# Performance work log

Hardware: AMD Instinct MI355X
Metric: run time of the kernel (lower is better)

## Reference

```python
import jax, jax.numpy as jnp
import numpy as np

B, S, D_MODEL, H = 4, 2048, 1024, 16
DEPTH = D_MODEL // H  # 64


def setup_inputs() -> dict:
    key = jax.random.key(0)
    ks = jax.random.split(key, 12)
    inp = {
        "v": jax.random.normal(ks[0], (B, S, D_MODEL), jnp.float32),
        "k": jax.random.normal(ks[1], (B, S, D_MODEL), jnp.float32),
        "q": jax.random.normal(ks[2], (B, S, D_MODEL), jnp.float32),
        "mask": jnp.zeros((B, 1, 1, S), jnp.int32),  # unused by the layer
        # Dense(d_model) params (glorot-ish scale)
        "wq": jax.random.normal(ks[3], (D_MODEL, D_MODEL), jnp.float32) / np.sqrt(D_MODEL),
        "bq": jnp.zeros((D_MODEL,), jnp.float32),
        "wk": jax.random.normal(ks[4], (D_MODEL, D_MODEL), jnp.float32) / np.sqrt(D_MODEL),
        "bk": jnp.zeros((D_MODEL,), jnp.float32),
        "wv": jax.random.normal(ks[5], (D_MODEL, D_MODEL), jnp.float32) / np.sqrt(D_MODEL),
        "bv": jnp.zeros((D_MODEL,), jnp.float32),
        # global attention weights: [max_seq_len, 1], stddev=0.1
        "gqw": 0.1 * jax.random.normal(ks[6], (S, 1), jnp.float32),
        "gkw": 0.1 * jax.random.normal(ks[7], (S, 1), jnp.float32),
        "wo": jax.random.normal(ks[8], (D_MODEL, D_MODEL), jnp.float32) / np.sqrt(D_MODEL),
        "bo": jnp.zeros((D_MODEL,), jnp.float32),
    }
    return inp


def _split_heads(x):
    # [B, S, D] -> [B, H, S, depth]
    Bc = x.shape[0]
    return x.reshape(Bc, -1, H, DEPTH).transpose(0, 2, 1, 3)


def reference(v, k, q, mask, wq, bq, wk, bk, wv, bv, gqw, gkw, wo, bo):
    # QKV projections
    qh = _split_heads(q @ wq + bq)  # [B, H, S, depth]
    kh = _split_heads(k @ wk + bk)
    vh = _split_heads(v @ wv + bv)
    # Fastformer additive attention: mul -> seq-sum -> mul -> seq-sum -> mul -> add
    qh = qh * gqw                          # gqw [S,1] broadcasts over [B,H,S,depth]
    gq = jnp.sum(qh, axis=2, keepdims=True)  # global query [B,H,1,depth]
    kh = kh * gq * gkw
    gk = jnp.sum(kh, axis=2, keepdims=True)  # global key [B,H,1,depth]
    out = vh * gk + qh                       # [B,H,S,depth]
    # merge heads and output projection
    out = out.transpose(0, 2, 1, 3).reshape(out.shape[0], -1, D_MODEL)
    return out @ wo + bo
```

## Files before the change

### kernel.cpp

```cpp
#include <hip/hip_runtime.h>

#define DM 1024
#define BATCH 4
#define SEQ 2048
#define M_TOT (BATCH*SEQ)

typedef unsigned short ushort_t;
typedef __bf16 bf16x8 __attribute__((ext_vector_type(8)));
typedef float f32x4 __attribute__((ext_vector_type(4)));
typedef unsigned short u16x4 __attribute__((ext_vector_type(4)));
typedef unsigned short u16x8 __attribute__((ext_vector_type(8)));

__device__ __forceinline__ ushort_t f2bf(float f) {
  unsigned u = __builtin_bit_cast(unsigned, f);
  u = (u + 0x7fffu + ((u >> 16) & 1u)) >> 16;
  return (ushort_t)u;
}
__device__ __forceinline__ float bf2f(ushort_t h) {
  unsigned u = ((unsigned)h) << 16;
  return __builtin_bit_cast(float, u);
}

#define GLL(gp, lp)                                                            \
  __builtin_amdgcn_global_load_lds(                                            \
      (const __attribute__((address_space(1))) unsigned int*)(const void*)(gp),\
      (__attribute__((address_space(3))) unsigned int*)(void*)(lp), 16, 0, 0)

__global__ void k_reduce(const float* __restrict__ q, const float* __restrict__ k,
                         const float* __restrict__ v,
                         const float* __restrict__ gqw, const float* __restrict__ gkw,
                         float* __restrict__ pq, float* __restrict__ pk,
                         float* __restrict__ G,
                         ushort_t* __restrict__ qb, ushort_t* __restrict__ vb) {
  const int b = blockIdx.x, sc = blockIdx.y;
  const int d0 = threadIdx.x * 4;
  const int s0 = sc * 8;
  const size_t base = ((size_t)b * SEQ + s0) * DM + d0;
  float aq0 = 0.f, aq1 = 0.f, aq2 = 0.f, aq3 = 0.f;
  float ak0 = 0.f, ak1 = 0.f, ak2 = 0.f, ak3 = 0.f;
  float sgq = 0.f, sgk = 0.f;
#pragma unroll
  for (int i = 0; i < 8; ++i) {
    const float wq_ = gqw[s0 + i], wk_ = gkw[s0 + i];
    const size_t off = base + (size_t)i * DM;
    const float4 qv = *(const float4*)(q + off);
    const float4 kv = *(const float4*)(k + off);
    const float4 vv = *(const float4*)(v + off);
    aq0 += wq_ * qv.x; aq1 += wq_ * qv.y; aq2 += wq_ * qv.z; aq3 += wq_ * qv.w;
    ak0 += wk_ * kv.x; ak1 += wk_ * kv.y; ak2 += wk_ * kv.z; ak3 += wk_ * kv.w;
    u16x4 oq, ov;
    oq[0] = f2bf(wq_ * qv.x); oq[1] = f2bf(wq_ * qv.y);
    oq[2] = f2bf(wq_ * qv.z); oq[3] = f2bf(wq_ * qv.w);
    ov[0] = f2bf(vv.x); ov[1] = f2bf(vv.y); ov[2] = f2bf(vv.z); ov[3] = f2bf(vv.w);
    *(u16x4*)(qb + off) = oq;
    *(u16x4*)(vb + off) = ov;
    sgq += wq_; sgk += wk_;
  }
  const size_t po = ((size_t)(sc * BATCH + b) << 10) + d0;
  *(float4*)(pq + po) = make_float4(aq0, aq1, aq2, aq3);
  *(float4*)(pk + po) = make_float4(ak0, ak1, ak2, ak3);
  if (b == 0 && threadIdx.x == 0) {
    atomicAdd(&G[0], sgq);
    atomicAdd(&G[1], sgk);
  }
}

__global__ void k_rsum(const float* __restrict__ pq, const float* __restrict__ pk,
                       float* __restrict__ qr, float* __restrict__ kr) {
  const int b = blockIdx.x;
  const int d = blockIdx.y * 256 + threadIdx.x;
  const int sg = blockIdx.z;
  float aq = 0.f, ak = 0.f;
#pragma unroll 4
  for (int s = sg * 32; s < sg * 32 + 32; ++s) {
    const size_t po = ((size_t)(s * BATCH + b) << 10) + d;
    aq += pq[po];
    ak += pk[po];
  }
  atomicAdd(&qr[b * DM + d], aq);
  atomicAdd(&kr[b * DM + d], ak);
}

__global__ void k_gpart(const float* __restrict__ wq, const float* __restrict__ wk,
                        const float* __restrict__ qr, const float* __restrict__ kr,
                        float* __restrict__ qacc, float* __restrict__ kacc) {
  const int d = blockIdx.x * 256 + threadIdx.x;
  const int k0 = blockIdx.y * 32;
  __shared__ float sq[4][32], sk[4][32];
  if (threadIdx.x < 128) {
    const int b = threadIdx.x >> 5, kk = threadIdx.x & 31;
    sq[b][kk] = qr[b * DM + k0 + kk];
    sk[b][kk] = kr[b * DM + k0 + kk];
  }
  __syncthreads();
  float aq[4] = {0.f, 0.f, 0.f, 0.f}, ak[4] = {0.f, 0.f, 0.f, 0.f};
#pragma unroll 8
  for (int kk = 0; kk < 32; ++kk) {
    const float wqv = wq[(size_t)(k0 + kk) * DM + d];
    const float wkv = wk[(size_t)(k0 + kk) * DM + d];
#pragma unroll
    for (int b = 0; b < 4; ++b) {
      aq[b] += sq[b][kk] * wqv;
      ak[b] += sk[b][kk] * wkv;
    }
  }
#pragma unroll
  for (int b = 0; b < 4; ++b) {
    atomicAdd(&qacc[b * DM + d], aq[b]);
    atomicAdd(&kacc[b * DM + d], ak[b]);
  }
}

__global__ void k_gfin(const float* __restrict__ qacc, const float* __restrict__ kacc,
                       const float* __restrict__ bq, const float* __restrict__ bk,
                       const float* __restrict__ G, float* __restrict__ gk) {
  const int i = blockIdx.x * 256 + threadIdx.x;
  const int d = i & (DM - 1);
  const float gqv = qacc[i] + bq[d] * G[0];
  const float gkr = kacc[i] + bk[d] * G[1];
  gk[i] = gqv * gkr;
}

__global__ void k_conv(const float* __restrict__ x0, ushort_t* __restrict__ y0,
                       const float* __restrict__ x1, ushort_t* __restrict__ y1) {
  const float* x = blockIdx.y ? x1 : x0;
  ushort_t* y = blockIdx.y ? y1 : y0;
  size_t i = (size_t)blockIdx.x * 256 + threadIdx.x;
  const float4* p = (const float4*)x + i * 2;
  float4 a = p[0], b = p[1];
  u16x8 o;
  o[0] = f2bf(a.x); o[1] = f2bf(a.y); o[2] = f2bf(a.z); o[3] = f2bf(a.w);
  o[4] = f2bf(b.x); o[5] = f2bf(b.y); o[6] = f2bf(b.z); o[7] = f2bf(b.w);
  *(u16x8*)(y + i * 8) = o;
}

__global__ void k_trans(const float* __restrict__ W, ushort_t* __restrict__ T) {
  __shared__ float ls[32][33];
  const int bi = blockIdx.x, bj = blockIdx.y;
#pragma unroll
  for (int p = 0; p < 4; ++p) {
    int e = threadIdx.x + p * 256;
    int r = e >> 5, c = e & 31;
    ls[r][c] = W[(size_t)(bi * 32 + r) * DM + bj * 32 + c];
  }
  __syncthreads();
#pragma unroll
  for (int p = 0; p < 4; ++p) {
    int e = threadIdx.x + p * 256;
    int r = e >> 5, c = e & 31;
    T[(size_t)(bj * 32 + r) * DM + bi * 32 + c] = f2bf(ls[c][r]);
  }
}

__global__ void k_wog(const ushort_t* __restrict__ woT, const float* __restrict__ gk,
                      ushort_t* __restrict__ wogT) {
  const size_t i = (size_t)blockIdx.x * 256 + threadIdx.x;
  const size_t c = i * 8;
  const int j0 = (int)(c & (DM - 1));
  const int b = (int)(c >> 20);
  u16x8 wv = *(const u16x8*)(woT + (c & ((1u << 20) - 1)));
  const float4 g0 = *(const float4*)(gk + b * DM + j0);
  const float4 g1 = *(const float4*)(gk + b * DM + j0 + 4);
  float g[8] = {g0.x, g0.y, g0.z, g0.w, g1.x, g1.y, g1.z, g1.w};
  u16x8 o;
#pragma unroll
  for (int j = 0; j < 8; ++j) o[j] = f2bf(bf2f(wv[j]) * g[j]);
  *(u16x8*)(wogT + i * 8) = o;
}

__global__ void k_bias(const float* __restrict__ wo, const float* __restrict__ bq,
                       const float* __restrict__ bv, const float* __restrict__ gk,
                       float* __restrict__ qbias, float* __restrict__ vbias) {
  const int n = blockIdx.x * 256 + threadIdx.x;
  const int k0 = blockIdx.y * 32;
  float aq = 0.f, av[4] = {0.f, 0.f, 0.f, 0.f};
  for (int kk = 0; kk < 32; ++kk) {
    const float w = wo[(size_t)(k0 + kk) * DM + n];
    aq += bq[k0 + kk] * w;
    const float bw = bv[k0 + kk] * w;
#pragma unroll
    for (int b = 0; b < 4; ++b) av[b] += bw * gk[b * DM + k0 + kk];
  }
  atomicAdd(&qbias[n], aq);
#pragma unroll
  for (int b = 0; b < 4; ++b) atomicAdd(&vbias[b * DM + n], av[b]);
}

template <int MODE, int NT>
__global__ __launch_bounds__(512, 1)
void k_pipe(const ushort_t* __restrict__ A0, const ushort_t* __restrict__ B0,
            const ushort_t* __restrict__ A1, const ushort_t* __restrict__ B1,
            const float* __restrict__ gqw, const float* __restrict__ qbias,
            const float* __restrict__ vbias, const float* __restrict__ bo,
            void* __restrict__ OutV) {
  __shared__ __align__(16) ushort_t lsA[3][256 * 64];
  __shared__ __align__(16) ushort_t lsB[3][128 * 64];
  const int tid = threadIdx.x;
  const int w = tid >> 6, lane = tid & 63;
  const int m0 = blockIdx.x * 256, n0 = blockIdx.y * 128;
  const int b = (MODE == 0) ? (m0 >> 11) : 0;
  const int wr = w >> 2, wc = w & 3;

  const ushort_t *Aq, *Bq, *Av = nullptr, *Bv = nullptr;
  if constexpr (MODE == 0) {
    Aq = A0; Bq = B0; Av = A1; Bv = B1 + (size_t)b * (DM * DM);
  } else {
    const int z = blockIdx.z;
    Aq = z ? A1 + (size_t)(z - 1) * (DM * DM) : A0;
    Bq = z ? B1 : B0;
  }

  const int subrow = lane >> 3;
  const int srcslot = (lane & 7) ^ subrow;
  size_t offA[4], offB[2];
#pragma unroll
  for (int p = 0; p < 4; ++p) {
    const int row = (4 * w + p) * 8 + subrow;
    offA[p] = (size_t)(m0 + row) * DM + srcslot * 8;
  }
#pragma unroll
  for (int p = 0; p < 2; ++p) {
    const int row = (2 * w + p) * 8 + subrow;
    offB[p] = (size_t)(n0 + row) * DM + srcslot * 8;
  }

  const int g = lane >> 4, l7 = lane & 7, l15 = lane & 15;
  int aoff[2][8], boff[2][2];
#pragma unroll
  for (int kh = 0; kh < 2; ++kh) {
#pragma unroll
    for (int i = 0; i < 8; ++i) {
      const int ra = wr * 128 + i * 16 + l15;
      aoff[kh][i] = ra * 64 + (((kh * 4 + g) ^ l7) * 8);
    }
#pragma unroll
    for (int j = 0; j < 2; ++j) {
      const int rb = wc * 32 + j * 16 + l15;
      boff[kh][j] = rb * 64 + (((kh * 4 + g) ^ l7) * 8);
    }
  }

  f32x4 acc[8][2];
#pragma unroll
  for (int i = 0; i < 8; ++i)
#pragma unroll
    for (int j = 0; j < 2; ++j) acc[i][j] = (f32x4){0.f, 0.f, 0.f, 0.f};

  auto SRC = [&](int tt, const ushort_t*& Ab, const ushort_t*& Bb, int& k0) {
    if (MODE == 0 && tt >= NT / 2) { Ab = Av; Bb = Bv; k0 = (tt - NT / 2) * 64; }
    else                           { Ab = Aq; Bb = Bq; k0 = tt * 64; }
  };
  auto STAGE_H0 = [&](int tt, int buf) {
    const ushort_t *Ab, *Bb; int k0; SRC(tt, Ab, Bb, k0);
    GLL(Ab + offA[0] + k0, &lsA[buf][(4 * w + 0) * 512]);
    GLL(Ab + offA[1] + k0, &lsA[buf][(4 * w + 1) * 512]);
    GLL(Bb + offB[0] + k0, &lsB[buf][(2 * w + 0) * 512]);
  };
  auto STAGE_H1 = [&](int tt, int buf) {
    const ushort_t *Ab, *Bb; int k0; SRC(tt, Ab, Bb, k0);
    GLL(Ab + offA[2] + k0, &lsA[buf][(4 * w + 2) * 512]);
    GLL(Ab + offA[3] + k0, &lsA[buf][(4 * w + 3) * 512]);
    GLL(Bb + offB[1] + k0, &lsB[buf][(2 * w + 1) * 512]);
  };
  auto READF = [&](bf16x8 (&av)[8], bf16x8 (&bv)[2], int cur, int kh) {
#pragma unroll
    for (int i = 0; i < 8; ++i) av[i] = *(const bf16x8*)(&lsA[cur][aoff[kh][i]]);
#pragma unroll
    for (int j = 0; j < 2; ++j) bv[j] = *(const bf16x8*)(&lsB[cur][boff[kh][j]]);
  };
  auto DOMFMA = [&](bf16x8 (&av)[8], bf16x8 (&bv)[2]) {
    __builtin_amdgcn_s_setprio(1);
#pragma unroll
    for (int i = 0; i < 8; ++i)
#pragma unroll
      for (int j = 0; j < 2; ++j)
        acc[i][j] = __builtin_amdgcn_mfma_f32_16x16x32_bf16(av[i], bv[j], acc[i][j], 0, 0, 0);
    __builtin_amdgcn_s_setprio(0);
  };

  bf16x8 avA[8], bvA[2], avB[8], bvB[2];

  STAGE_H0(0, 0); STAGE_H1(0, 0);
  STAGE_H0(1, 1); STAGE_H1(1, 1);
  asm volatile("s_waitcnt vmcnt(6)" ::: "memory");
  __builtin_amdgcn_s_barrier();
  READF(avA, bvA, 0, 0);

#pragma unroll 1
  for (int t = 0; t < NT; ++t) {
    const int cur = t % 3, nb = (t + 2) % 3, nxt = (t + 1) % 3;
    READF(avB, bvB, cur, 1);
    if (t + 2 < NT) STAGE_H0(t + 2, nb);
    DOMFMA(avA, bvA);
    if (t + 1 < NT) {
      if (t + 2 < NT) { asm volatile("s_waitcnt vmcnt(3)\n\ts_barrier" ::: "memory"); }
      else            { asm volatile("s_waitcnt vmcnt(0)\n\ts_barrier" ::: "memory"); }
      READF(avA, bvA, nxt, 0);
      if (t + 2 < NT) STAGE_H1(t + 2, nb);
    }
    DOMFMA(avB, bvB);
  }

  const int lr = (lane >> 4) * 4, lc = lane & 15;
  const int rbase = m0 + wr * 128, cbase = n0 + wc * 32;
  if constexpr (MODE == 0) {
    float* Out = (float*)OutV;
#pragma unroll
    for (int j = 0; j < 2; ++j) {
      const int col = cbase + j * 16 + lc;
      const float qbn = qbias[col];
      const float cb = vbias[b * DM + col] + bo[col];
#pragma unroll
      for (int i = 0; i < 8; ++i)
#pragma unroll
        for (int r = 0; r < 4; ++r) {
          const int row = rbase + i * 16 + lr + r;
          Out[(size_t)row * DM + col] = acc[i][j][r] + gqw[row & (SEQ - 1)] * qbn + cb;
        }
    }
  } else {
    ushort_t* Out = (ushort_t*)OutV + (size_t)blockIdx.z * (DM * DM);
#pragma unroll
    for (int j = 0; j < 2; ++j) {
      const int col = cbase + j * 16 + lc;
#pragma unroll
      for (int i = 0; i < 8; ++i)
#pragma unroll
        for (int r = 0; r < 4; ++r) {
          const int row = rbase + i * 16 + lr + r;
          Out[(size_t)row * DM + col] = f2bf(acc[i][j][r]);
        }
    }
  }
}

extern "C" void kernel_launch(void* const* d_in, const int* in_sizes, int n_in,
                              void* d_out, int out_size, void* d_ws, size_t ws_size,
                              hipStream_t stream) {
  const float* v   = (const float*)d_in[0];
  const float* k   = (const float*)d_in[1];
  const float* q   = (const float*)d_in[2];
  const float* wq  = (const float*)d_in[4];
  const float* bq  = (const float*)d_in[5];
  const float* wk  = (const float*)d_in[6];
  const float* bk  = (const float*)d_in[7];
  const float* wv  = (const float*)d_in[8];
  const float* bv  = (const float*)d_in[9];
  const float* gqw = (const float*)d_in[10];
  const float* gkw = (const float*)d_in[11];
  const float* wo  = (const float*)d_in[12];
  const float* bo  = (const float*)d_in[13];
  float* out = (float*)d_out;
  float* wsf = (float*)d_ws;

  float* qr    = wsf + 0;
  float* kr    = wsf + 4096;
  float* qacc  = wsf + 8192;
  float* kacc  = wsf + 12288;
  float* G     = wsf + 16384;
  float* qbias = wsf + 16640;
  float* vbias = wsf + 17664;
  float* gk    = wsf + 21760;
  ushort_t* b16  = (ushort_t*)((char*)d_ws + (1 << 17));
  ushort_t* qb   = b16;
  ushort_t* vb   = qb + (size_t)M_TOT * DM;
  ushort_t* wqB  = vb + (size_t)M_TOT * DM;
  ushort_t* wvB  = wqB + (size_t)DM * DM;
  ushort_t* woT  = wvB + (size_t)DM * DM;
  ushort_t* WqoT = woT + (size_t)DM * DM;
  ushort_t* WvbT = WqoT + (size_t)DM * DM;
  ushort_t* wogT = (ushort_t*)out;
  float* pq = out + (1 << 22);
  float* pk = pq + (1 << 20);

  hipMemsetAsync(d_ws, 0, 21760 * sizeof(float), stream);

  k_conv<<<dim3((DM * DM / 8) / 256, 2), 256, 0, stream>>>(wq, wqB, wv, wvB);
  k_trans<<<dim3(32, 32), 256, 0, stream>>>(wo, woT);

  k_reduce<<<dim3(BATCH, SEQ / 8), 256, 0, stream>>>(q, k, v, gqw, gkw, pq, pk, G, qb, vb);
  k_rsum<<<dim3(BATCH, DM / 256, 8), 256, 0, stream>>>(pq, pk, qr, kr);

  k_gpart<<<dim3(DM / 256, DM / 32), 256, 0, stream>>>(wq, wk, qr, kr, qacc, kacc);
  k_gfin<<<(BATCH * DM) / 256, 256, 0, stream>>>(qacc, kacc, bq, bk, G, gk);

  k_wog<<<(BATCH * DM * DM / 8) / 256, 256, 0, stream>>>(woT, gk, wogT);
  k_bias<<<dim3(DM / 256, DM / 32), 256, 0, stream>>>(wo, bq, bv, gk, qbias, vbias);

  k_pipe<1, 16><<<dim3(4, 8, 5), 512, 0, stream>>>(
      woT, wqB, wogT, wvB, nullptr, nullptr, nullptr, nullptr, WqoT);

  k_pipe<0, 32><<<dim3(M_TOT / 256, DM / 128), 512, 0, stream>>>(
      qb, WqoT, vb, WvbT, gqw, qbias, vbias, bo, out);
}
```

Measured before the change: 123.1 us.

## Rework warp tiling in k_pipe and halve weight-fold GEMM tile to BM=128

The weight-fold GEMM (MODE 1) now uses a 128-row tile instead of 256, doubling its grid from 160 to 320 blocks so more CUs have work. Its vmcnt wait counts are adjusted to match the fewer loads per stage. The warp layout also changes for both modes: MODE 0 goes from 2x4 warps with 128x32 subtiles to 4x2 warps with 64x64 subtiles. That gives more balanced A/B fragment reuse per warp and fewer LDS reads per MFMA. The cost is a smaller tile with less reuse in MODE 1, and a different register and LDS access pattern in the main GEMM.

Result: slower. 128.9 us (+4.7%).

```diff
diff --git a/kernel.cpp b/kernel.cpp
--- a/kernel.cpp
+++ b/kernel.cpp
@@ -193,13 +193,17 @@
             const float* __restrict__ gqw, const float* __restrict__ qbias,
             const float* __restrict__ vbias, const float* __restrict__ bo,
             void* __restrict__ OutV) {
-  __shared__ __align__(16) ushort_t lsA[3][256 * 64];
+  constexpr int BM  = (MODE == 0) ? 256 : 128;
+  constexpr int NI  = (MODE == 0) ? 4 : 2;
+  constexpr int ACH = BM / 64;
+  __shared__ __align__(16) ushort_t lsA[3][BM * 64];
   __shared__ __align__(16) ushort_t lsB[3][128 * 64];
   const int tid = threadIdx.x;
   const int w = tid >> 6, lane = tid & 63;
-  const int m0 = blockIdx.x * 256, n0 = blockIdx.y * 128;
+  const int m0 = blockIdx.x * BM, n0 = blockIdx.y * 128;
   const int b = (MODE == 0) ? (m0 >> 11) : 0;
-  const int wr = w >> 2, wc = w & 3;
+  const int wr = (MODE == 0) ? (w >> 1) : (w >> 2);
+  const int wc = (MODE == 0) ? (w & 1) : (w & 3);
 
   const ushort_t *Aq, *Bq, *Av = nullptr, *Bv = nullptr;
   if constexpr (MODE == 0) {
@@ -212,10 +216,10 @@
 
   const int subrow = lane >> 3;
   const int srcslot = (lane & 7) ^ subrow;
-  size_t offA[4], offB[2];
-#pragma unroll
-  for (int p = 0; p < 4; ++p) {
-    const int row = (4 * w + p) * 8 + subrow;
+  size_t offA[ACH], offB[2];
+#pragma unroll
+  for (int p = 0; p < ACH; ++p) {
+    const int row = (ACH * w + p) * 8 + subrow;
     offA[p] = (size_t)(m0 + row) * DM + srcslot * 8;
   }
 #pragma unroll
@@ -225,26 +229,26 @@
   }
 
   const int g = lane >> 4, l7 = lane & 7, l15 = lane & 15;
-  int aoff[2][8], boff[2][2];
+  int aoff[2][4], boff[2][NI];
 #pragma unroll
   for (int kh = 0; kh < 2; ++kh) {
 #pragma unroll
-    for (int i = 0; i < 8; ++i) {
-      const int ra = wr * 128 + i * 16 + l15;
+    for (int i = 0; i < 4; ++i) {
+      const int ra = wr * 64 + i * 16 + l15;
       aoff[kh][i] = ra * 64 + (((kh * 4 + g) ^ l7) * 8);
     }
 #pragma unroll
-    for (int j = 0; j < 2; ++j) {
-      const int rb = wc * 32 + j * 16 + l15;
+    for (int j = 0; j < NI; ++j) {
+      const int rb = wc * (NI * 16) + j * 16 + l15;
       boff[kh][j] = rb * 64 + (((kh * 4 + g) ^ l7) * 8);
     }
   }
 
-  f32x4 acc[8][2];
-#pragma unroll
-  for (int i = 0; i < 8; ++i)
-#pragma unroll
-    for (int j = 0; j < 2; ++j) acc[i][j] = (f32x4){0.f, 0.f, 0.f, 0.f};
+  f32x4 acc[4][NI];
+#pragma unroll
+  for (int i = 0; i < 4; ++i)
+#pragma unroll
+    for (int j = 0; j < NI; ++j) acc[i][j] = (f32x4){0.f, 0.f, 0.f, 0.f};
 
   auto SRC = [&](int tt, const ushort_t*& Ab, const ushort_t*& Bb, int& k0) {
     if (MODE == 0 && tt >= NT / 2) { Ab = Av; Bb = Bv; k0 = (tt - NT / 2) * 64; }
@@ -252,37 +256,40 @@
   };
   auto STAGE_H0 = [&](int tt, int buf) {
     const ushort_t *Ab, *Bb; int k0; SRC(tt, Ab, Bb, k0);
-    GLL(Ab + offA[0] + k0, &lsA[buf][(4 * w + 0) * 512]);
-    GLL(Ab + offA[1] + k0, &lsA[buf][(4 * w + 1) * 512]);
+#pragma unroll
+    for (int p = 0; p < ACH / 2; ++p)
+      GLL(Ab + offA[p] + k0, &lsA[buf][(ACH * w + p) * 512]);
     GLL(Bb + offB[0] + k0, &lsB[buf][(2 * w + 0) * 512]);
   };
   auto STAGE_H1 = [&](int tt, int buf) {
     const ushort_t *Ab, *Bb; int k0; SRC(tt, Ab, Bb, k0);
-    GLL(Ab + offA[2] + k0, &lsA[buf][(4 * w + 2) * 512]);
-    GLL(Ab + offA[3] + k0, &lsA[buf][(4 * w + 3) * 512]);
+#pragma unroll
+    for (int p = ACH / 2; p < ACH; ++p)
+      GLL(Ab + offA[p] + k0, &lsA[buf][(ACH * w + p) * 512]);
     GLL(Bb + offB[1] + k0, &lsB[buf][(2 * w + 1) * 512]);
   };
-  auto READF = [&](bf16x8 (&av)[8], bf16x8 (&bv)[2], int cur, int kh) {
-#pragma unroll
-    for (int i = 0; i < 8; ++i) av[i] = *(const bf16x8*)(&lsA[cur][aoff[kh][i]]);
-#pragma unroll
-    for (int j = 0; j < 2; ++j) bv[j] = *(const bf16x8*)(&lsB[cur][boff[kh][j]]);
+  auto READF = [&](bf16x8 (&av)[4], bf16x8 (&bv)[NI], int cur, int kh) {
+#pragma unroll
+    for (int i = 0; i < 4; ++i) av[i] = *(const bf16x8*)(&lsA[cur][aoff[kh][i]]);
+#pragma unroll
+    for (int j = 0; j < NI; ++j) bv[j] = *(const bf16x8*)(&lsB[cur][boff[kh][j]]);
   };
-  auto DOMFMA = [&](bf16x8 (&av)[8], bf16x8 (&bv)[2]) {
+  auto DOMFMA = [&](bf16x8 (&av)[4], bf16x8 (&bv)[NI]) {
     __builtin_amdgcn_s_setprio(1);
 #pragma unroll
-    for (int i = 0; i < 8; ++i)
-#pragma unroll
-      for (int j = 0; j < 2; ++j)
+    for (int i = 0; i < 4; ++i)
+#pragma unroll
+      for (int j = 0; j < NI; ++j)
         acc[i][j] = __builtin_amdgcn_mfma_f32_16x16x32_bf16(av[i], bv[j], acc[i][j], 0, 0, 0);
     __builtin_amdgcn_s_setprio(0);
   };
 
-  bf16x8 avA[8], bvA[2], avB[8], bvB[2];
+  bf16x8 avA[4], bvA[NI], avB[4], bvB[NI];
 
   STAGE_H0(0, 0); STAGE_H1(0, 0);
   STAGE_H0(1, 1); STAGE_H1(1, 1);
-  asm volatile("s_waitcnt vmcnt(6)" ::: "memory");
+  if constexpr (MODE == 0) { asm volatile("s_waitcnt vmcnt(6)" ::: "memory"); }
+  else                     { asm volatile("s_waitcnt vmcnt(4)" ::: "memory"); }
   __builtin_amdgcn_s_barrier();
   READF(avA, bvA, 0, 0);
 
@@ -293,8 +300,12 @@
     if (t + 2 < NT) STAGE_H0(t + 2, nb);
     DOMFMA(avA, bvA);
     if (t + 1 < NT) {
-      if (t + 2 < NT) { asm volatile("s_waitcnt vmcnt(3)\n\ts_barrier" ::: "memory"); }
-      else            { asm volatile("s_waitcnt vmcnt(0)\n\ts_barrier" ::: "memory"); }
+      if (t + 2 < NT) {
+        if constexpr (MODE == 0) { asm volatile("s_waitcnt vmcnt(3)\n\ts_barrier" ::: "memory"); }
+        else                     { asm volatile("s_waitcnt vmcnt(2)\n\ts_barrier" ::: "memory"); }
+      } else {
+        asm volatile("s_waitcnt vmcnt(0)\n\ts_barrier" ::: "memory");
+      }
       READF(avA, bvA, nxt, 0);
       if (t + 2 < NT) STAGE_H1(t + 2, nb);
     }
@@ -302,16 +313,16 @@
   }
 
   const int lr = (lane >> 4) * 4, lc = lane & 15;
-  const int rbase = m0 + wr * 128, cbase = n0 + wc * 32;
+  const int rbase = m0 + wr * 64, cbase = n0 + wc * (NI * 16);
   if constexpr (MODE == 0) {
     float* Out = (float*)OutV;
 #pragma unroll
-    for (int j = 0; j < 2; ++j) {
+    for (int j = 0; j < NI; ++j) {
       const int col = cbase + j * 16 + lc;
       const float qbn = qbias[col];
       const float cb = vbias[b * DM + col] + bo[col];
 #pragma unroll
-      for (int i = 0; i < 8; ++i)
+      for (int i = 0; i < 4; ++i)
 #pragma unroll
         for (int r = 0; r < 4; ++r) {
           const int row = rbase + i * 16 + lr + r;
@@ -321,10 +332,10 @@
   } else {
     ushort_t* Out = (ushort_t*)OutV + (size_t)blockIdx.z * (DM * DM);
 #pragma unroll
-    for (int j = 0; j < 2; ++j) {
+    for (int j = 0; j < NI; ++j) {
       const int col = cbase + j * 16 + lc;
 #pragma unroll
-      for (int i = 0; i < 8; ++i)
+      for (int i = 0; i < 4; ++i)
 #pragma unroll
         for (int r = 0; r < 4; ++r) {
           const int row = rbase + i * 16 + lr + r;
@@ -387,7 +398,7 @@
   k_wog<<<(BATCH * DM * DM / 8) / 256, 256, 0, stream>>>(woT, gk, wogT);
   k_bias<<<dim3(DM / 256, DM / 32), 256, 0, stream>>>(wo, bq, bv, gk, qbias, vbias);
 
-  k_pipe<1, 16><<<dim3(4, 8, 5), 512, 0, stream>>>(
+  k_pipe<1, 16><<<dim3(8, 8, 5), 512, 0, stream>>>(
       woT, wqB, wogT, wvB, nullptr, nullptr, nullptr, nullptr, WqoT);
 
   k_pipe<0, 32><<<dim3(M_TOT / 256, DM / 128), 512, 0, stream>>>(
```
